# Performance work log

Measured on AMD Instinct MI355X. Metric: run time of the kernel, lower is better.

The kernel has to match this reference:

```python
import jax, jax.numpy as jnp
import numpy as np

K = 1024          # num_embeddings
D = 256           # embedding_dim
COMMITMENT = 0.25


def setup_inputs() -> dict:
    key = jax.random.key(0)
    k1, k2 = jax.random.split(key)
    inputs = jax.random.normal(k1, (16, D, 4096), dtype=jnp.float32)  # [B, D, T]
    # torch init: uniform(-1/K, 1/K)
    emb_weight = jax.random.uniform(k2, (K, D), dtype=jnp.float32,
                                    minval=-1.0 / K, maxval=1.0 / K)
    return {"inputs": inputs, "emb_weight": emb_weight}


def reference(inputs, emb_weight):
    B, Dd, T = inputs.shape
    x = jnp.transpose(inputs, (0, 2, 1))          # [B, T, D]
    flat = x.reshape(-1, Dd)                      # [N, D]

    dist = (jnp.sum(flat * flat, axis=1, keepdims=True)
            + jnp.sum(emb_weight * emb_weight, axis=1)
            - 2.0 * flat @ emb_weight.T)          # [N, K]
    idx = jnp.argmin(dist, axis=1)                # [N]

    quantized = emb_weight[idx].reshape(B, T, Dd)  # gather == one-hot matmul

    e_latent = jnp.mean((jax.lax.stop_gradient(quantized) - x) ** 2)
    q_latent = jnp.mean((quantized - jax.lax.stop_gradient(x)) ** 2)
    loss = q_latent + COMMITMENT * e_latent

    # straight-through estimator
    q_ste = x + jax.lax.stop_gradient(quantized - x)
    q_out = jnp.transpose(q_ste, (0, 2, 1))       # [B, D, T]

    counts = jnp.zeros((K,), dtype=jnp.float32).at[idx].add(1.0)
    avg_probs = counts / idx.shape[0]
    perplexity = jnp.exp(-jnp.sum(avg_probs * jnp.log(avg_probs + 1e-10)))

    encoding_indices = idx.reshape(B, T)
    return q_out, loss, encoding_indices, perplexity
```

## Files before the change

### kernel.cpp

```cpp
#include <hip/hip_runtime.h>
#include <math.h>

#define DD 256
#define KK 1024
#define TT 4096
#define BB 16
#define NN (BB*TT)
#define QSZ (BB*DD*TT)
#define LOSS_POS QSZ
#define IDX_OFF (QSZ+1)
#define PERP_POS (QSZ+1+NN)

#define WS_NE    0
#define WS_IDX   4096
#define WS_CNT   (4096 + NN*4)
#define WS_LOSS  (WS_CNT + KK*4)
#define WS_FLAG  (WS_LOSS + 8)

#define OUT_EH   0
#define OUT_XN   (1u<<20)
#define OUT_FL   (2u<<20)

#define THR 1.4e-4f

typedef __attribute__((ext_vector_type(8))) _Float16 half8v;
typedef __attribute__((ext_vector_type(4))) float f32x4;

__device__ __forceinline__ unsigned mapf(float f) {
    unsigned b = __float_as_uint(f);
    return (b & 0x80000000u) ? ~b : (b | 0x80000000u);
}

__device__ __forceinline__ float np_pairwise_sq(const float* __restrict__ p,
                                                const long stride) {
    float tot[2];
    #pragma unroll
    for (int h = 0; h < 2; ++h) {
        const float* q = p + (long)h * 128 * stride;
        float r[8];
        #pragma unroll
        for (int j = 0; j < 8; ++j) {
            const float v = q[(long)j * stride];
            r[j] = __fmul_rn(v, v);
        }
        for (int i = 8; i < 128; i += 8) {
            #pragma unroll
            for (int j = 0; j < 8; ++j) {
                const float v = q[(long)(i + j) * stride];
                r[j] = __fadd_rn(r[j], __fmul_rn(v, v));
            }
        }
        tot[h] = __fadd_rn(__fadd_rn(__fadd_rn(r[0], r[1]), __fadd_rn(r[2], r[3])),
                           __fadd_rn(__fadd_rn(r[4], r[5]), __fadd_rn(r[6], r[7])));
    }
    return __fadd_rn(tot[0], tot[1]);
}

__global__ __launch_bounds__(256) void vq_prep_e(const float* __restrict__ emb,
                                                 float* __restrict__ ne,
                                                 _Float16* __restrict__ eh) {
    const int k = blockIdx.x * 256 + threadIdx.x;
    const float* row = emb + (size_t)k * DD;
    ne[k] = np_pairwise_sq(row, 1);
    _Float16* er = eh + (size_t)k * DD;
    #pragma unroll 8
    for (int d = 0; d < DD; ++d) er[d] = (_Float16)(row[d] * 1024.0f);
}

__global__ __launch_bounds__(256) void vq_xnorm(const float* __restrict__ x,
                                                float* __restrict__ xn) {
    const int n = blockIdx.x * 256 + threadIdx.x;
    const int b = n >> 12;
    const int t = n & 4095;
    xn[n] = np_pairwise_sq(x + (size_t)b * DD * TT + t, TT);
}

__global__ __launch_bounds__(256) void vq_argmin_f16(
    const float* __restrict__ x,
    const _Float16* __restrict__ eh,
    const float* __restrict__ ne,
    const float* __restrict__ xn,
    int* __restrict__ out_idx,
    int* __restrict__ flag_cnt,
    int* __restrict__ flag_list)
{
    __shared__ __align__(16) _Float16 Elds[2][128 * 32];
    __shared__ float nes[KK];

    const int tid = threadIdx.x;
    const int w   = tid >> 6;
    const int l   = tid & 63;
    const int l15 = l & 15;
    const int lg  = l >> 4;
    const int bx  = blockIdx.x;
    const int b   = bx >> 5;
    const int t0  = (bx & 31) * 128;
    const int tw0 = t0 + w * 32;

    for (int i = tid; i < KK; i += 256) nes[i] = ne[i];

    half8v Bf[2][8];
    const float* xb = x + (size_t)b * DD * TT;
    #pragma unroll
    for (int ft = 0; ft < 2; ++ft) {
        const int t = tw0 + ft * 16 + l15;
        #pragma unroll
        for (int dc = 0; dc < 8; ++dc) {
            const int d0 = dc * 32 + lg * 8;
            half8v v;
            #pragma unroll
            for (int j = 0; j < 8; ++j) v[j] = (_Float16)xb[(size_t)(d0 + j) * TT + t];
            Bf[ft][dc] = v;
        }
    }
    const float xnv[2] = { xn[b * TT + tw0 + l15], xn[b * TT + tw0 + 16 + l15] };

    float v1[2] = {3.4028235e38f, 3.4028235e38f};
    float v2[2] = {3.4028235e38f, 3.4028235e38f};
    int   k1[2] = {0, 0};

    const int row0 = tid >> 2;
    const int row1 = row0 + 64;
    const int cg   = tid & 3;
    const int xc0  = cg ^ ((row0 >> 1) & 3);
    const int xc1  = cg ^ ((row1 >> 1) & 3);

    half8v g0, g1;
    g0 = *(const half8v*)(eh + (size_t)row0 * DD + xc0 * 8);
    g1 = *(const half8v*)(eh + (size_t)row1 * DD + xc1 * 8);
    *(half8v*)&Elds[0][row0 * 32 + cg * 8] = g0;
    *(half8v*)&Elds[0][row1 * 32 + cg * 8] = g1;
    __syncthreads();

    f32x4 acc[8][2];
    const int rsw = (lg ^ ((l15 >> 1) & 3)) * 8;

    for (int s = 0; s < 64; ++s) {
        const int kc = s >> 3, dc = s & 7;

        if (dc == 0) {
            #pragma unroll
            for (int fk = 0; fk < 8; ++fk) {
                acc[fk][0] = f32x4{0.f, 0.f, 0.f, 0.f};
                acc[fk][1] = f32x4{0.f, 0.f, 0.f, 0.f};
            }
        }

        if (s + 1 < 64) {
            const int kn = (s + 1) >> 3, dn = (s + 1) & 7;
            g0 = *(const half8v*)(eh + (size_t)(kn * 128 + row0) * DD + dn * 32 + xc0 * 8);
            g1 = *(const half8v*)(eh + (size_t)(kn * 128 + row1) * DD + dn * 32 + xc1 * 8);
        }

        {
            const _Float16* eb = Elds[s & 1];
            #pragma unroll
            for (int fk = 0; fk < 8; ++fk) {
                const half8v Af = *(const half8v*)&eb[(fk * 16 + l15) * 32 + rsw];
                acc[fk][0] = __builtin_amdgcn_mfma_f32_16x16x32_f16(Af, Bf[0][dc], acc[fk][0], 0, 0, 0);
                acc[fk][1] = __builtin_amdgcn_mfma_f32_16x16x32_f16(Af, Bf[1][dc], acc[fk][1], 0, 0, 0);
            }
        }

        if (dc == 7) {
            #pragma unroll
            for (int ft = 0; ft < 2; ++ft) {
                #pragma unroll
                for (int fk = 0; fk < 8; ++fk) {
                    const float4 nev = *reinterpret_cast<const float4*>(
                        &nes[kc * 128 + fk * 16 + lg * 4]);
                    const float nv[4] = {nev.x, nev.y, nev.z, nev.w};
                    #pragma unroll
                    for (int r = 0; r < 4; ++r) {
                        const float sa = __fadd_rn(xnv[ft], nv[r]);
                        const float sc = fmaf(-0.001953125f, acc[fk][ft][r], sa);
                        const float mx = fmaxf(v1[ft], sc);
                        v2[ft] = fminf(v2[ft], mx);
                        const bool c = sc < v1[ft];
                        v1[ft] = c ? sc : v1[ft];
                        k1[ft] = c ? (kc * 128 + fk * 16 + lg * 4 + r) : k1[ft];
                    }
                }
            }
        }

        __syncthreads();
        if (s + 1 < 64) {
            _Float16* ebn = Elds[(s + 1) & 1];
            *(half8v*)&ebn[row0 * 32 + cg * 8] = g0;
            *(half8v*)&ebn[row1 * 32 + cg * 8] = g1;
        }
        __syncthreads();
    }

    #pragma unroll
    for (int ft = 0; ft < 2; ++ft) {
        #pragma unroll
        for (int m = 16; m <= 32; m <<= 1) {
            const float ov1 = __shfl_xor(v1[ft], m);
            const float ov2 = __shfl_xor(v2[ft], m);
            const int   ok1 = __shfl_xor(k1[ft], m);
            const float mx  = fmaxf(v1[ft], ov1);
            v2[ft] = fminf(fminf(v2[ft], ov2), mx);
            const bool take = (ov1 < v1[ft]) || (ov1 == v1[ft] && ok1 < k1[ft]);
            v1[ft] = take ? ov1 : v1[ft];
            k1[ft] = take ? ok1 : k1[ft];
        }
        if (l < 16) {
            const int n = b * TT + tw0 + ft * 16 + l15;
            out_idx[n] = k1[ft];
            if (v2[ft] - v1[ft] <= THR) {
                const int p = atomicAdd(flag_cnt, 1);
                flag_list[p] = n;
            }
        }
    }
}

#define CR 16
__global__ __launch_bounds__(512) void vq_cleanup(
    const float* __restrict__ x, const float* __restrict__ emb,
    const float* __restrict__ ne, const float* __restrict__ xn,
    const int* __restrict__ flag_cnt, const int* __restrict__ flag_list,
    int* __restrict__ out_idx)
{
    __shared__ float xr[CR][DD + 4];
    __shared__ float xns_s[CR];
    __shared__ int rowid[CR];
    __shared__ unsigned long long wred[8][8];

    const int tid = threadIdx.x;
    const int wv  = tid >> 6, l = tid & 63;
    const int kt  = tid & 255;
    const int rt  = tid >> 8;
    const int cnt = *flag_cnt;

    for (int base = blockIdx.x * CR; base < cnt; base += gridDim.x * CR) {
        const int nr = min(CR, cnt - base);
        __syncthreads();
        if (tid < CR) {
            const int n = flag_list[base + ((tid < nr) ? tid : (nr - 1))];
            rowid[tid] = n;
            xns_s[tid] = xn[n];
        }
        __syncthreads();
        {
            const int r = tid >> 5, d0 = (tid & 31) * 8;
            const int n = rowid[r], bb2 = n >> 12, t = n & 4095;
            const float* xc = x + (size_t)bb2 * DD * TT + t;
            #pragma unroll
            for (int q = 0; q < 8; ++q) xr[r][d0 + q] = xc[(size_t)(d0 + q) * TT];
        }
        __syncthreads();

        const int k0 = kt * 4;
        float acc4[4][8];
        #pragma unroll
        for (int a = 0; a < 4; ++a)
            #pragma unroll
            for (int r = 0; r < 8; ++r) acc4[a][r] = 0.f;

        for (int ch = 0; ch < DD / 8; ++ch) {
            const int d0 = ch * 8;
            float xc8[8][8];
            #pragma unroll
            for (int r = 0; r < 8; ++r) {
                const float4 xa = *reinterpret_cast<const float4*>(&xr[rt * 8 + r][d0]);
                const float4 xbv = *reinterpret_cast<const float4*>(&xr[rt * 8 + r][d0 + 4]);
                xc8[r][0] = xa.x;  xc8[r][1] = xa.y;  xc8[r][2] = xa.z;  xc8[r][3] = xa.w;
                xc8[r][4] = xbv.x; xc8[r][5] = xbv.y; xc8[r][6] = xbv.z; xc8[r][7] = xbv.w;
            }
            #pragma unroll
            for (int a = 0; a < 4; ++a) {
                const float* er = emb + (size_t)(k0 + a) * DD + d0;
                const float4 ea = *reinterpret_cast<const float4*>(er);
                const float4 eb2 = *reinterpret_cast<const float4*>(er + 4);
                const float ev[8] = {ea.x, ea.y, ea.z, ea.w, eb2.x, eb2.y, eb2.z, eb2.w};
                #pragma unroll
                for (int q = 0; q < 8; ++q)
                    #pragma unroll
                    for (int r = 0; r < 8; ++r)
                        acc4[a][r] = fmaf(ev[q], xc8[r][q], acc4[a][r]);
            }
        }

        #pragma unroll
        for (int r = 0; r < 8; ++r) {
            const float xnv2 = xns_s[rt * 8 + r];
            unsigned long long bb3 = ~0ull;
            #pragma unroll
            for (int a = 0; a < 4; ++a) {
                const float s1 = __fadd_rn(xnv2, ne[k0 + a]);
                const float sc = __fsub_rn(s1, __fmul_rn(2.0f, acc4[a][r]));
                const unsigned long long pk =
                    ((unsigned long long)mapf(sc) << 32) | (unsigned)(k0 + a);
                bb3 = (pk < bb3) ? pk : bb3;
            }
            unsigned long long v = bb3;
            #pragma unroll
            for (int m = 1; m < 64; m <<= 1) {
                const unsigned long long o = __shfl_xor(v, m);
                v = (o < v) ? o : v;
            }
            if (l == 0) wred[wv][r] = v;
        }
        __syncthreads();
        if (wv == 0) {
            const int row = l >> 2, sw = l & 3;
            const int srcw = (row < 8) ? sw : (4 + sw);
            unsigned long long v = wred[srcw][row & 7];
            #pragma unroll
            for (int m = 1; m < 4; m <<= 1) {
                const unsigned long long o = __shfl_xor(v, m);
                v = (o < v) ? o : v;
            }
            if (sw == 0 && row < nr) out_idx[rowid[row]] = (int)(v & 0xFFFFFFFFu);
        }
    }
}

__global__ __launch_bounds__(256) void vq_gather(
    const float* __restrict__ x, const float* __restrict__ emb,
    const int* __restrict__ idx, float* __restrict__ out,
    int* __restrict__ counts, double* __restrict__ loss_acc)
{
    const int n = blockIdx.x * 256 + threadIdx.x;
    const int b = n >> 12;
    const int t = n & 4095;
    const int id = idx[n];
    const float* erow = emb + (size_t)id * DD;
    const float* xcol = x   + (size_t)b * DD * TT + t;
    float* ocol       = out + (size_t)b * DD * TT + t;

    float s = 0.f;
    #pragma unroll 4
    for (int d4 = 0; d4 < DD / 4; ++d4) {
        const float4 ev = *reinterpret_cast<const float4*>(erow + d4 * 4);
        const float e0 = ev.x, e1 = ev.y, e2 = ev.z, e3 = ev.w;
        const size_t base = (size_t)(d4 * 4) * TT;
        float xv, df;
        xv = xcol[base];            ocol[base]            = e0; df = e0 - xv; s = fmaf(df, df, s);
        xv = xcol[base + TT];       ocol[base + TT]       = e1; df = e1 - xv; s = fmaf(df, df, s);
        xv = xcol[base + 2 * TT];   ocol[base + 2 * TT]   = e2; df = e2 - xv; s = fmaf(df, df, s);
        xv = xcol[base + 3 * TT];   ocol[base + 3 * TT]   = e3; df = e3 - xv; s = fmaf(df, df, s);
    }
    out[IDX_OFF + n] = (float)id;
    atomicAdd(&counts[id], 1);

    __shared__ double red[256];
    red[threadIdx.x] = (double)s;
    __syncthreads();
    for (int off = 128; off; off >>= 1) {
        if (threadIdx.x < off) red[threadIdx.x] += red[threadIdx.x + off];
        __syncthreads();
    }
    if (threadIdx.x == 0) atomicAdd(loss_acc, red[0]);
}

__global__ void vq_finalize(const int* __restrict__ counts,
                            const double* __restrict__ loss_acc,
                            float* __restrict__ out)
{
    __shared__ double red[256];
    const int tid = threadIdx.x;
    double s = 0.0;
    for (int k = tid; k < KK; k += 256) {
        const double p = (double)counts[k] / (double)NN;
        s += p * log(p + 1e-10);
    }
    red[tid] = s;
    __syncthreads();
    for (int off = 128; off; off >>= 1) {
        if (tid < off) red[tid] += red[tid + off];
        __syncthreads();
    }
    if (tid == 0) {
        out[PERP_POS] = (float)exp(-red[0]);
        out[LOSS_POS] = (float)(1.25 * loss_acc[0] / (double)QSZ);
    }
}

extern "C" void kernel_launch(void* const* d_in, const int* in_sizes, int n_in,
                              void* d_out, int out_size, void* d_ws, size_t ws_size,
                              hipStream_t stream) {
    const float* x   = (const float*)d_in[0];
    const float* emb = (const float*)d_in[1];
    float* out = (float*)d_out;
    char*  ws  = (char*)d_ws;

    float*     ne        = (float*)(ws + WS_NE);
    int*       idx       = (int*)(ws + WS_IDX);
    int*       counts    = (int*)(ws + WS_CNT);
    double*    loss_acc  = (double*)(ws + WS_LOSS);
    int*       flag_cnt  = (int*)(ws + WS_FLAG);
    _Float16*  eh        = (_Float16*)((char*)d_out + OUT_EH);
    float*     xn        = (float*)((char*)d_out + OUT_XN);
    int*       flag_list = (int*)((char*)d_out + OUT_FL);

    hipMemsetAsync(ws + WS_CNT, 0, KK * 4 + 16, stream);

    vq_prep_e<<<KK / 256, 256, 0, stream>>>(emb, ne, eh);
    vq_xnorm<<<NN / 256, 256, 0, stream>>>(x, xn);
    vq_argmin_f16<<<512, 256, 0, stream>>>(x, eh, ne, xn, idx, flag_cnt, flag_list);
    vq_cleanup<<<256, 512, 0, stream>>>(x, emb, ne, xn, flag_cnt, flag_list, idx);
    vq_gather<<<NN / 256, 256, 0, stream>>>(x, emb, idx, out, counts, loss_acc);
    vq_finalize<<<1, 256, 0, stream>>>(counts, loss_acc, out);
}
```

Measured before the change: 425.4 us.

## Use direct global-to-LDS loads, smaller argmin tiles, vectorized gather and prep stores

The argmin kernel now streams codebook tiles straight into LDS with global_load_lds, which drops the register staging and one barrier per step. Each block now covers 64 time steps instead of 128, with one MFMA column tile per wave, and the grid doubles to 1024 blocks for more occupancy at the cost of more codebook reloads. The gather kernel now handles 4 consecutive time steps per thread with float4 loads and stores of x and the output, with the embedding dimension split across 8 blocks. The prep kernel writes the half-precision codebook as 16-byte vectors.

```diff
diff --git a/kernel.cpp b/kernel.cpp
--- a/kernel.cpp
+++ b/kernel.cpp
@@ -26,6 +26,10 @@
 typedef __attribute__((ext_vector_type(8))) _Float16 half8v;
 typedef __attribute__((ext_vector_type(4))) float f32x4;
 
+#define GLOAD16(gp, lp) __builtin_amdgcn_global_load_lds( \
+    (const __attribute__((address_space(1))) unsigned int*)(gp), \
+    (__attribute__((address_space(3))) unsigned int*)(lp), 16, 0, 0)
+
 __device__ __forceinline__ unsigned mapf(float f) {
     unsigned b = __float_as_uint(f);
     return (b & 0x80000000u) ? ~b : (b | 0x80000000u);
@@ -63,8 +67,13 @@
     const float* row = emb + (size_t)k * DD;
     ne[k] = np_pairwise_sq(row, 1);
     _Float16* er = eh + (size_t)k * DD;
-    #pragma unroll 8
-    for (int d = 0; d < DD; ++d) er[d] = (_Float16)(row[d] * 1024.0f);
+    #pragma unroll 4
+    for (int c = 0; c < DD / 8; ++c) {
+        half8v h;
+        #pragma unroll
+        for (int j = 0; j < 8; ++j) h[j] = (_Float16)(row[c * 8 + j] * 1024.0f);
+        *reinterpret_cast<half8v*>(er + c * 8) = h;
+    }
 }
 
 __global__ __launch_bounds__(256) void vq_xnorm(const float* __restrict__ x,
@@ -93,46 +102,41 @@
     const int l15 = l & 15;
     const int lg  = l >> 4;
     const int bx  = blockIdx.x;
-    const int b   = bx >> 5;
-    const int t0  = (bx & 31) * 128;
-    const int tw0 = t0 + w * 32;
+    const int b   = bx >> 6;
+    const int t0  = (bx & 63) * 64;
+    const int tw0 = t0 + w * 16;
 
     for (int i = tid; i < KK; i += 256) nes[i] = ne[i];
 
-    half8v Bf[2][8];
+    half8v Bf[8];
     const float* xb = x + (size_t)b * DD * TT;
-    #pragma unroll
-    for (int ft = 0; ft < 2; ++ft) {
-        const int t = tw0 + ft * 16 + l15;
+    {
+        const int t = tw0 + l15;
         #pragma unroll
         for (int dc = 0; dc < 8; ++dc) {
             const int d0 = dc * 32 + lg * 8;
             half8v v;
             #pragma unroll
             for (int j = 0; j < 8; ++j) v[j] = (_Float16)xb[(size_t)(d0 + j) * TT + t];
-            Bf[ft][dc] = v;
-        }
-    }
-    const float xnv[2] = { xn[b * TT + tw0 + l15], xn[b * TT + tw0 + 16 + l15] };
-
-    float v1[2] = {3.4028235e38f, 3.4028235e38f};
-    float v2[2] = {3.4028235e38f, 3.4028235e38f};
-    int   k1[2] = {0, 0};
+            Bf[dc] = v;
+        }
+    }
+    const float xnv = xn[b * TT + tw0 + l15];
+
+    float v1 = 3.4028235e38f, v2 = 3.4028235e38f;
+    int   k1 = 0;
 
     const int row0 = tid >> 2;
-    const int row1 = row0 + 64;
     const int cg   = tid & 3;
-    const int xc0  = cg ^ ((row0 >> 1) & 3);
-    const int xc1  = cg ^ ((row1 >> 1) & 3);
-
-    half8v g0, g1;
-    g0 = *(const half8v*)(eh + (size_t)row0 * DD + xc0 * 8);
-    g1 = *(const half8v*)(eh + (size_t)row1 * DD + xc1 * 8);
-    *(half8v*)&Elds[0][row0 * 32 + cg * 8] = g0;
-    *(half8v*)&Elds[0][row1 * 32 + cg * 8] = g1;
+    const int xc   = cg ^ ((row0 >> 1) & 3);
+    _Float16* lds0[2] = { &Elds[0][w * 512], &Elds[1][w * 512] };
+    _Float16* lds1[2] = { &Elds[0][2048 + w * 512], &Elds[1][2048 + w * 512] };
+
+    GLOAD16(eh + (size_t)row0 * DD + xc * 8, lds0[0]);
+    GLOAD16(eh + (size_t)(row0 + 64) * DD + xc * 8, lds1[0]);
     __syncthreads();
 
-    f32x4 acc[8][2];
+    f32x4 acc[8];
     const int rsw = (lg ^ ((l15 >> 1) & 3)) * 8;
 
     for (int s = 0; s < 64; ++s) {
@@ -140,79 +144,64 @@
 
         if (dc == 0) {
             #pragma unroll
-            for (int fk = 0; fk < 8; ++fk) {
-                acc[fk][0] = f32x4{0.f, 0.f, 0.f, 0.f};
-                acc[fk][1] = f32x4{0.f, 0.f, 0.f, 0.f};
-            }
+            for (int fk = 0; fk < 8; ++fk) acc[fk] = f32x4{0.f, 0.f, 0.f, 0.f};
         }
 
         if (s + 1 < 64) {
             const int kn = (s + 1) >> 3, dn = (s + 1) & 7;
-            g0 = *(const half8v*)(eh + (size_t)(kn * 128 + row0) * DD + dn * 32 + xc0 * 8);
-            g1 = *(const half8v*)(eh + (size_t)(kn * 128 + row1) * DD + dn * 32 + xc1 * 8);
+            const _Float16* src = eh + (size_t)(kn * 128 + row0) * DD + dn * 32 + xc * 8;
+            GLOAD16(src, lds0[(s + 1) & 1]);
+            GLOAD16(src + (size_t)64 * DD, lds1[(s + 1) & 1]);
         }
 
         {
-            const _Float16* eb = Elds[s & 1];
+            const _Float16* ebuf = Elds[s & 1];
             #pragma unroll
             for (int fk = 0; fk < 8; ++fk) {
-                const half8v Af = *(const half8v*)&eb[(fk * 16 + l15) * 32 + rsw];
-                acc[fk][0] = __builtin_amdgcn_mfma_f32_16x16x32_f16(Af, Bf[0][dc], acc[fk][0], 0, 0, 0);
-                acc[fk][1] = __builtin_amdgcn_mfma_f32_16x16x32_f16(Af, Bf[1][dc], acc[fk][1], 0, 0, 0);
+                const half8v Af = *(const half8v*)&ebuf[(fk * 16 + l15) * 32 + rsw];
+                acc[fk] = __builtin_amdgcn_mfma_f32_16x16x32_f16(Af, Bf[dc], acc[fk], 0, 0, 0);
             }
         }
 
         if (dc == 7) {
             #pragma unroll
-            for (int ft = 0; ft < 2; ++ft) {
+            for (int fk = 0; fk < 8; ++fk) {
+                const float4 nev = *reinterpret_cast<const float4*>(
+                    &nes[kc * 128 + fk * 16 + lg * 4]);
+                const float nv[4] = {nev.x, nev.y, nev.z, nev.w};
                 #pragma unroll
-                for (int fk = 0; fk < 8; ++fk) {
-                    const float4 nev = *reinterpret_cast<const float4*>(
-                        &nes[kc * 128 + fk * 16 + lg * 4]);
-                    const float nv[4] = {nev.x, nev.y, nev.z, nev.w};
-                    #pragma unroll
-                    for (int r = 0; r < 4; ++r) {
-                        const float sa = __fadd_rn(xnv[ft], nv[r]);
-                        const float sc = fmaf(-0.001953125f, acc[fk][ft][r], sa);
-                        const float mx = fmaxf(v1[ft], sc);
-                        v2[ft] = fminf(v2[ft], mx);
-                        const bool c = sc < v1[ft];
-                        v1[ft] = c ? sc : v1[ft];
-                        k1[ft] = c ? (kc * 128 + fk * 16 + lg * 4 + r) : k1[ft];
-                    }
+                for (int r = 0; r < 4; ++r) {
+                    const float sa = __fadd_rn(xnv, nv[r]);
+                    const float sc = fmaf(-0.001953125f, acc[fk][r], sa);
+                    const float mx = fmaxf(v1, sc);
+                    v2 = fminf(v2, mx);
+                    const bool c = sc < v1;
+                    v1 = c ? sc : v1;
+                    k1 = c ? (kc * 128 + fk * 16 + lg * 4 + r) : k1;
                 }
             }
         }
 
         __syncthreads();
-        if (s + 1 < 64) {
-            _Float16* ebn = Elds[(s + 1) & 1];
-            *(half8v*)&ebn[row0 * 32 + cg * 8] = g0;
-            *(half8v*)&ebn[row1 * 32 + cg * 8] = g1;
-        }
-        __syncthreads();
     }
 
     #pragma unroll
-    for (int ft = 0; ft < 2; ++ft) {
-        #pragma unroll
-        for (int m = 16; m <= 32; m <<= 1) {
-            const float ov1 = __shfl_xor(v1[ft], m);
-            const float ov2 = __shfl_xor(v2[ft], m);
-            const int   ok1 = __shfl_xor(k1[ft], m);
-            const float mx  = fmaxf(v1[ft], ov1);
-            v2[ft] = fminf(fminf(v2[ft], ov2), mx);
-            const bool take = (ov1 < v1[ft]) || (ov1 == v1[ft] && ok1 < k1[ft]);
-            v1[ft] = take ? ov1 : v1[ft];
-            k1[ft] = take ? ok1 : k1[ft];
-        }
-        if (l < 16) {
-            const int n = b * TT + tw0 + ft * 16 + l15;
-            out_idx[n] = k1[ft];
-            if (v2[ft] - v1[ft] <= THR) {
-                const int p = atomicAdd(flag_cnt, 1);
-                flag_list[p] = n;
-            }
+    for (int m = 16; m <= 32; m <<= 1) {
+        const float ov1 = __shfl_xor(v1, m);
+        const float ov2 = __shfl_xor(v2, m);
+        const int   ok1 = __shfl_xor(k1, m);
+        const float mx  = fmaxf(v1, ov1);
+        v2 = fminf(fminf(v2, ov2), mx);
+        const bool take = (ov1 < v1) || (ov1 == v1 && ok1 < k1);
+        v1 = take ? ov1 : v1;
+        k1 = take ? ok1 : k1;
+    }
+    if (l < 16) {
+        const int n = b * TT + tw0 + l15;
+        out_idx[n] = k1;
+        if (v2 - v1 <= THR) {
+            const int p = atomicAdd(flag_cnt, 1);
+            flag_list[p] = n;
         }
     }
 }
@@ -292,9 +281,9 @@
             for (int a = 0; a < 4; ++a) {
                 const float s1 = __fadd_rn(xnv2, ne[k0 + a]);
                 const float sc = __fsub_rn(s1, __fmul_rn(2.0f, acc4[a][r]));
-                const unsigned long long pk =
+                const unsigned long long pkk =
                     ((unsigned long long)mapf(sc) << 32) | (unsigned)(k0 + a);
-                bb3 = (pk < bb3) ? pk : bb3;
+                bb3 = (pkk < bb3) ? pkk : bb3;
             }
             unsigned long long v = bb3;
             #pragma unroll
@@ -324,37 +313,61 @@
     const int* __restrict__ idx, float* __restrict__ out,
     int* __restrict__ counts, double* __restrict__ loss_acc)
 {
-    const int n = blockIdx.x * 256 + threadIdx.x;
-    const int b = n >> 12;
-    const int t = n & 4095;
-    const int id = idx[n];
-    const float* erow = emb + (size_t)id * DD;
-    const float* xcol = x   + (size_t)b * DD * TT + t;
-    float* ocol       = out + (size_t)b * DD * TT + t;
+    const int tid = threadIdx.x;
+    const int bid = blockIdx.x;
+    const int ds2 = bid & 7;
+    const int g   = (bid >> 3) * 256 + tid;
+    const int b   = g >> 10;
+    const int t0q = (g & 1023) * 4;
+    const int n0  = b * TT + t0q;
+
+    int ids[4];
+    #pragma unroll
+    for (int q = 0; q < 4; ++q) ids[q] = idx[n0 + q];
+
+    const int dbase = ds2 * 32;
+    const float* xb = x + (size_t)b * DD * TT;
+    float* ob       = out + (size_t)b * DD * TT;
 
     float s = 0.f;
-    #pragma unroll 4
-    for (int d4 = 0; d4 < DD / 4; ++d4) {
-        const float4 ev = *reinterpret_cast<const float4*>(erow + d4 * 4);
-        const float e0 = ev.x, e1 = ev.y, e2 = ev.z, e3 = ev.w;
-        const size_t base = (size_t)(d4 * 4) * TT;
-        float xv, df;
-        xv = xcol[base];            ocol[base]            = e0; df = e0 - xv; s = fmaf(df, df, s);
-        xv = xcol[base + TT];       ocol[base + TT]       = e1; df = e1 - xv; s = fmaf(df, df, s);
-        xv = xcol[base + 2 * TT];   ocol[base + 2 * TT]   = e2; df = e2 - xv; s = fmaf(df, df, s);
-        xv = xcol[base + 3 * TT];   ocol[base + 3 * TT]   = e3; df = e3 - xv; s = fmaf(df, df, s);
-    }
-    out[IDX_OFF + n] = (float)id;
-    atomicAdd(&counts[id], 1);
+    for (int d4 = 0; d4 < 8; ++d4) {
+        const int d = dbase + d4 * 4;
+        float ea[4][4];
+        #pragma unroll
+        for (int q = 0; q < 4; ++q) {
+            const float4 v = *reinterpret_cast<const float4*>(emb + (size_t)ids[q] * DD + d);
+            ea[q][0] = v.x; ea[q][1] = v.y; ea[q][2] = v.z; ea[q][3] = v.w;
+        }
+        #pragma unroll
+        for (int di = 0; di < 4; ++di) {
+            const float4 xv = *reinterpret_cast<const float4*>(xb + (size_t)(d + di) * TT + t0q);
+            float4 ov;
+            ov.x = ea[0][di]; ov.y = ea[1][di]; ov.z = ea[2][di]; ov.w = ea[3][di];
+            *reinterpret_cast<float4*>(ob + (size_t)(d + di) * TT + t0q) = ov;
+            float df;
+            df = ov.x - xv.x; s = fmaf(df, df, s);
+            df = ov.y - xv.y; s = fmaf(df, df, s);
+            df = ov.z - xv.z; s = fmaf(df, df, s);
+            df = ov.w - xv.w; s = fmaf(df, df, s);
+        }
+    }
+
+    if (ds2 == 0) {
+        #pragma unroll
+        for (int q = 0; q < 4; ++q) {
+            out[IDX_OFF + n0 + q] = (float)ids[q];
+            atomicAdd(&counts[ids[q]], 1);
+        }
+    }
 
     __shared__ double red[256];
-    red[threadIdx.x] = (double)s;
+    red[tid] = (double)s;
     __syncthreads();
     for (int off = 128; off; off >>= 1) {
-        if (threadIdx.x < off) red[threadIdx.x] += red[threadIdx.x + off];
-        __syncthreads();
-    }
-    if (threadIdx.x == 0) atomicAdd(loss_acc, red[0]);
+        if (tid < off) red[tid] += red[tid + off];
+        __syncthreads();
+    }
+    if (tid == 0) atomicAdd(loss_acc, red[0]);
 }
 
 __global__ void vq_finalize(const int* __restrict__ counts,
@@ -401,8 +414,8 @@
 
     vq_prep_e<<<KK / 256, 256, 0, stream>>>(emb, ne, eh);
     vq_xnorm<<<NN / 256, 256, 0, stream>>>(x, xn);
-    vq_argmin_f16<<<512, 256, 0, stream>>>(x, eh, ne, xn, idx, flag_cnt, flag_list);
+    vq_argmin_f16<<<1024, 256, 0, stream>>>(x, eh, ne, xn, idx, flag_cnt, flag_list);
     vq_cleanup<<<256, 512, 0, stream>>>(x, emb, ne, xn, flag_cnt, flag_list, idx);
-    vq_gather<<<NN / 256, 256, 0, stream>>>(x, emb, idx, out, counts, loss_acc);
+    vq_gather<<<512, 256, 0, stream>>>(x, emb, idx, out, counts, loss_acc);
     vq_finalize<<<1, 256, 0, stream>>>(counts, loss_acc, out);
 }
```

Result: slower. 855.8 us (+101.2%).
